# Performance work log

Hardware: AMD Instinct MI355X
Metric: run time of the kernel (lower is better)

Reference implementation:

```python
import jax, jax.numpy as jnp
import numpy as np
from jax import lax

DIM, HEADS, HIDDEN = 384, 6, 1536
B, D, H, W = 2, 14, 14, 14
LN_EPS = 1e-5


def setup_inputs() -> dict:
    key = jax.random.key(0)
    ks = jax.random.split(key, 8)
    s = 0.02
    return {
        "x": jax.random.normal(ks[0], (B, DIM, D, H, W), jnp.float32),
        "conv_w": jax.random.normal(ks[1], (DIM, 1, 3, 3, 3), jnp.float32) * s,
        "conv_b": jnp.zeros((DIM,), jnp.float32),
        "ln1_w": jnp.ones((DIM,), jnp.float32),
        "ln1_b": jnp.zeros((DIM,), jnp.float32),
        "qkv_w": jax.random.normal(ks[2], (3 * DIM, DIM), jnp.float32) * s,
        "proj_w": jax.random.normal(ks[3], (DIM, DIM), jnp.float32) * s,
        "proj_b": jnp.zeros((DIM,), jnp.float32),
        "ln2_w": jnp.ones((DIM,), jnp.float32),
        "ln2_b": jnp.zeros((DIM,), jnp.float32),
        "fc1_w": jax.random.normal(ks[4], (HIDDEN, DIM), jnp.float32) * s,
        "fc1_b": jnp.zeros((HIDDEN,), jnp.float32),
        "fc2_w": jax.random.normal(ks[5], (DIM, HIDDEN), jnp.float32) * s,
        "fc2_b": jnp.zeros((DIM,), jnp.float32),
    }


def _layernorm(x, w, b):
    mu = jnp.mean(x, axis=-1, keepdims=True)
    var = jnp.var(x, axis=-1, keepdims=True)
    return (x - mu) * lax.rsqrt(var + LN_EPS) * w + b


def reference(x, conv_w, conv_b, ln1_w, ln1_b, qkv_w, proj_w, proj_b,
              ln2_w, ln2_b, fc1_w, fc1_b, fc2_w, fc2_b):
    Bn, C = x.shape[0], x.shape[1]
    Dd, Hh, Ww = x.shape[2], x.shape[3], x.shape[4]
    # depthwise conv3d positional embedding (groups=dim), padding=1
    pos = lax.conv_general_dilated(
        x, conv_w, window_strides=(1, 1, 1), padding="SAME",
        feature_group_count=C,
        dimension_numbers=("NCDHW", "OIDHW", "NCDHW"))
    x = x + pos + conv_b[None, :, None, None, None] * 0 + conv_b[None, :, None, None, None]
    # fix: bias belongs to conv output only once
    x = x - conv_b[None, :, None, None, None]
    N = Dd * Hh * Ww
    t = x.reshape(Bn, C, N).transpose(0, 2, 1)  # [B, N, C]

    # attention
    hd = C // HEADS
    scale = hd ** -0.5
    tn = _layernorm(t, ln1_w, ln1_b)
    qkv = tn @ qkv_w.T  # [B, N, 3C]
    qkv = qkv.reshape(Bn, N, 3, HEADS, hd).transpose(2, 0, 3, 1, 4)
    q, k, v = qkv[0], qkv[1], qkv[2]  # [B, H, N, hd]
    attn = jax.nn.softmax(jnp.einsum("bhnd,bhmd->bhnm", q, k) * scale, axis=-1)
    o = jnp.einsum("bhnm,bhmd->bhnd", attn, v)
    o = o.transpose(0, 2, 1, 3).reshape(Bn, N, C)
    t = t + o @ proj_w.T + proj_b

    # MLP (exact GELU, matching torch nn.GELU default)
    tn2 = _layernorm(t, ln2_w, ln2_b)
    h = jax.nn.gelu(tn2 @ fc1_w.T + fc1_b, approximate=False)
    t = t + h @ fc2_w.T + fc2_b

    return t.transpose(0, 2, 1).reshape(Bn, C, Dd, Hh, Ww)
```

## Files before the change

### kernel.cpp

```cpp
#include <hip/hip_runtime.h>
#include <hip/hip_bf16.h>
#include <math.h>

#define DIM 384
#define HEADS 6
#define HIDDEN 1536
#define NTOK 2744
#define BATCH 2
#define MTOT (BATCH * NTOK)
#define KSPLIT 4
#define NQT 22
#define CEXP 0.18033688f

typedef __bf16 bf16x8 __attribute__((ext_vector_type(8)));
typedef __bf16 bf16x4 __attribute__((ext_vector_type(4)));
typedef float  f32x4  __attribute__((ext_vector_type(4)));

#define F_GELU  1
#define F_RESID 2
#define F_BF16  4
#define F_QKV   8
#define F_TRANS 16

__device__ __forceinline__ void gll16(const void* g, void* l) {
    __builtin_amdgcn_global_load_lds(
        (const __attribute__((address_space(1))) unsigned int*)g,
        (__attribute__((address_space(3))) unsigned int*)l, 16, 0, 0);
}

__global__ void k_conv(const float* __restrict__ x, const float* __restrict__ cw,
                       float* __restrict__ t,
                       const float* __restrict__ w0, const float* __restrict__ w1,
                       const float* __restrict__ w2, const float* __restrict__ w3,
                       __bf16* o0, __bf16* o1, __bf16* o2, __bf16* o3) {
    int bid = blockIdx.x;
    if (bid >= 528) {
        int i = (bid - 528) * 256 + threadIdx.x;
        const float* s; __bf16* d; int off;
        if (i < 110592)      { s = w0; d = o0; off = i; }
        else if (i < 147456) { s = w1; d = o1; off = i - 110592; }
        else if (i < 294912) { s = w2; d = o2; off = i - 147456; }
        else                 { s = w3; d = o3; off = i - 294912; }
        float4 v = ((const float4*)s)[off];
        bf16x4 bb = { (__bf16)v.x, (__bf16)v.y, (__bf16)v.z, (__bf16)v.w };
        *(bf16x4*)(d + (size_t)off * 4) = bb;
        return;
    }
    int nb = bid % 11, rest = bid / 11;
    int cb = rest % 24, b = rest / 24;
    int c0 = cb * 16;
    int n = nb * 256 + threadIdx.x;
    if (n >= NTOK) return;
    int d = n / 196, r = n % 196, h = r / 14, w = r % 14;
    const float* xb = x + ((size_t)b * DIM + c0) * NTOK;
    float acc[16];
    #pragma unroll
    for (int c = 0; c < 16; c++) acc[c] = xb[(size_t)c * NTOK + n];
    #pragma unroll
    for (int kd = 0; kd < 3; kd++) {
        int dd = d + kd - 1;
        if (dd < 0 || dd >= 14) continue;
        #pragma unroll
        for (int kh = 0; kh < 3; kh++) {
            int hh = h + kh - 1;
            if (hh < 0 || hh >= 14) continue;
            #pragma unroll
            for (int kw = 0; kw < 3; kw++) {
                int ww = w + kw - 1;
                if (ww < 0 || ww >= 14) continue;
                int np = (dd * 14 + hh) * 14 + ww;
                int tap = kd * 9 + kh * 3 + kw;
                #pragma unroll
                for (int c = 0; c < 16; c++)
                    acc[c] = fmaf(cw[(c0 + c) * 27 + tap], xb[(size_t)c * NTOK + np], acc[c]);
            }
        }
    }
    float* tp = t + (size_t)(b * NTOK + n) * DIM + c0;
    #pragma unroll
    for (int c = 0; c < 16; c += 4) {
        float4 v = { acc[c], acc[c + 1], acc[c + 2], acc[c + 3] };
        *(float4*)(tp + c) = v;
    }
}

__device__ __forceinline__ void ln_body(const float* __restrict__ in,
                                        __bf16* __restrict__ out,
                                        const float* __restrict__ w,
                                        const float* __restrict__ b) {
    int wid = threadIdx.x >> 6, lane = threadIdx.x & 63;
    int token = blockIdx.x * 4 + wid;
    const float* row = in + (size_t)token * DIM;
    float v[6], s = 0.f, s2 = 0.f;
    #pragma unroll
    for (int i = 0; i < 6; i++) {
        v[i] = row[lane + 64 * i];
        s += v[i]; s2 += v[i] * v[i];
    }
    #pragma unroll
    for (int m = 1; m < 64; m <<= 1) { s += __shfl_xor(s, m); s2 += __shfl_xor(s2, m); }
    float mu = s * (1.f / DIM);
    float rstd = rsqrtf(s2 * (1.f / DIM) - mu * mu + 1e-5f);
    __bf16* orow = out + (size_t)token * DIM;
    #pragma unroll
    for (int i = 0; i < 6; i++) {
        int c = lane + 64 * i;
        orow[c] = (__bf16)((v[i] - mu) * rstd * w[c] + b[c]);
    }
}
__global__ void k_ln1(const float* in, __bf16* out, const float* w, const float* b) {
    ln_body(in, out, w, b);
}
__global__ void k_ln2(const float* in, __bf16* out, const float* w, const float* b) {
    ln_body(in, out, w, b);
}

__device__ __forceinline__ void gemm12864_body(
    const __bf16* __restrict__ A, const __bf16* __restrict__ B,
    const float* __restrict__ bias, void* __restrict__ out,
    __bf16* __restrict__ vt_out, int M, int N, int K, int flags) {
    __shared__ __bf16 As[128][64];
    __shared__ __bf16 Bs[64][64];
    int tid = threadIdx.x, lane = tid & 63, wid = tid >> 6;
    int quad = lane >> 4, l16 = lane & 15;
    int wm = wid & 1, wn = wid >> 1;
    int m0 = blockIdx.y * 128, n0 = blockIdx.x * 64;
    int x7 = l16 & 7;

    auto stage = [&](int k0) {
        #pragma unroll
        for (int i = 0; i < 4; i++) {
            int c = i * 256 + tid;
            int row = c >> 3, cc = (c & 7) ^ (row & 7);
            int gm = m0 + row; if (gm > M - 1) gm = M - 1;
            gll16(A + (size_t)gm * K + k0 + cc * 8, &As[0][0] + (size_t)c * 8);
        }
        #pragma unroll
        for (int i = 0; i < 2; i++) {
            int c = i * 256 + tid;
            int row = c >> 3, cc = (c & 7) ^ (row & 7);
            gll16(B + (size_t)(n0 + row) * K + k0 + cc * 8, &Bs[0][0] + (size_t)c * 8);
        }
    };

    f32x4 acc[4][2] = {};
    int nk = K >> 6;
    for (int ki = 0; ki < nk; ki++) {
        if (ki) __syncthreads();
        stage(ki << 6);
        __syncthreads();
        #pragma unroll
        for (int s = 0; s < 2; s++) {
            bf16x8 a[4], b[2];
            #pragma unroll
            for (int i = 0; i < 4; i++)
                a[i] = *(bf16x8*)&As[wm * 64 + i * 16 + l16][(((s * 4 + quad) ^ x7)) * 8];
            #pragma unroll
            for (int j = 0; j < 2; j++)
                b[j] = *(bf16x8*)&Bs[wn * 32 + j * 16 + l16][(((s * 4 + quad) ^ x7)) * 8];
            #pragma unroll
            for (int i = 0; i < 4; i++)
                #pragma unroll
                for (int j = 0; j < 2; j++)
                    acc[i][j] = __builtin_amdgcn_mfma_f32_16x16x32_bf16(a[i], b[j], acc[i][j], 0, 0, 0);
        }
    }

    int colb = n0 + wn * 32;
    #pragma unroll
    for (int j = 0; j < 2; j++) {
        int col = colb + j * 16 + l16;
        float bv = bias ? bias[col] : 0.f;
        #pragma unroll
        for (int i = 0; i < 4; i++) {
            int row0 = m0 + wm * 64 + i * 16 + quad * 4;
            if (row0 >= M) continue;
            float v4[4];
            #pragma unroll
            for (int r = 0; r < 4; r++) {
                float v = acc[i][j][r] + bv;
                if (flags & F_GELU) v = 0.5f * v * (1.f + erff(v * 0.70710678f));
                if ((flags & F_QKV) && col < 384) v *= CEXP;
                v4[r] = v;
            }
            if ((flags & F_QKV) && col >= 768) {
                int b2 = row0 / NTOK, n2 = row0 - b2 * NTOK;
                bf16x4 pk = { (__bf16)v4[0], (__bf16)v4[1], (__bf16)v4[2], (__bf16)v4[3] };
                *(bf16x4*)(vt_out + ((size_t)(b2 * DIM + (col - 768))) * NTOK + n2) = pk;
            } else {
                #pragma unroll
                for (int r = 0; r < 4; r++)
                    ((__bf16*)out)[(size_t)(row0 + r) * N + col] = (__bf16)v4[r];
            }
        }
    }
}
__global__ __launch_bounds__(256) void k_qkv(const __bf16* A, const __bf16* B,
        void* out, __bf16* vt_out, int M, int N, int K) {
    gemm12864_body(A, B, nullptr, out, vt_out, M, N, K, F_QKV);
}
__global__ __launch_bounds__(256) void k_fc1(const __bf16* A, const __bf16* B,
        const float* bias, void* out, int M, int N, int K) {
    gemm12864_body(A, B, bias, out, nullptr, M, N, K, F_GELU | F_BF16);
}

__device__ __forceinline__ void gemm64_body(
    const __bf16* __restrict__ A, const __bf16* __restrict__ B,
    const float* __restrict__ bias, const float* __restrict__ resid,
    void* __restrict__ out, int M, int N, int K, int flags) {
    __shared__ __align__(16) char sm[17408];
    __bf16 (*As)[64] = (__bf16(*)[64])sm;
    __bf16 (*Bs)[64] = (__bf16(*)[64])(sm + 8192);
    float* Tt = (float*)sm;
    int tid = threadIdx.x, lane = tid & 63, wid = tid >> 6;
    int quad = lane >> 4, l16 = lane & 15;
    int wm = wid & 1, wn = wid >> 1;
    int m0 = blockIdx.y * 64, n0 = blockIdx.x * 64;
    int x7 = l16 & 7;

    auto stage = [&](int k0) {
        #pragma unroll
        for (int i = 0; i < 2; i++) {
            int c = i * 256 + tid;
            int row = c >> 3, cc = (c & 7) ^ (row & 7);
            int gm = m0 + row; if (gm > M - 1) gm = M - 1;
            gll16(A + (size_t)gm * K + k0 + cc * 8, &As[0][0] + (size_t)c * 8);
        }
        #pragma unroll
        for (int i = 0; i < 2; i++) {
            int c = i * 256 + tid;
            int row = c >> 3, cc = (c & 7) ^ (row & 7);
            gll16(B + (size_t)(n0 + row) * K + k0 + cc * 8, &Bs[0][0] + (size_t)c * 8);
        }
    };

    f32x4 acc[2][2] = {};
    int nk = K >> 6;
    for (int ki = 0; ki < nk; ki++) {
        if (ki) __syncthreads();
        stage(ki << 6);
        __syncthreads();
        #pragma unroll
        for (int s = 0; s < 2; s++) {
            bf16x8 a[2], b[2];
            #pragma unroll
            for (int i = 0; i < 2; i++)
                a[i] = *(bf16x8*)&As[wm * 32 + i * 16 + l16][(((s * 4 + quad) ^ x7)) * 8];
            #pragma unroll
            for (int j = 0; j < 2; j++)
                b[j] = *(bf16x8*)&Bs[wn * 32 + j * 16 + l16][(((s * 4 + quad) ^ x7)) * 8];
            #pragma unroll
            for (int i = 0; i < 2; i++)
                #pragma unroll
                for (int j = 0; j < 2; j++)
                    acc[i][j] = __builtin_amdgcn_mfma_f32_16x16x32_bf16(a[i], b[j], acc[i][j], 0, 0, 0);
        }
    }

    if (flags & F_TRANS) {
        #pragma unroll
        for (int half = 0; half < 2; half++) {
            __syncthreads();
            if (wn == half) {
                #pragma unroll
                for (int j = 0; j < 2; j++) {
                    int colL = j * 16 + l16;
                    int col = n0 + half * 32 + colL;
                    float bv = bias[col];
                    #pragma unroll
                    for (int i = 0; i < 2; i++) {
                        int rowL = wm * 32 + i * 16 + quad * 4;
                        float v4[4];
                        #pragma unroll
                        for (int r = 0; r < 4; r++) {
                            int rr = m0 + rowL + r; if (rr > M - 1) rr = M - 1;
                            v4[r] = acc[i][j][r] + bv + resid[(size_t)rr * N + col];
                        }
                        float4 pk = { v4[0], v4[1], v4[2], v4[3] };
                        *(float4*)&Tt[colL * 68 + rowL] = pk;
                    }
                }
            }
            __syncthreads();
            int c = tid >> 3, no = (tid & 7) * 8;
            int col = n0 + half * 32 + c;
            #pragma unroll
            for (int q2 = 0; q2 < 2; q2++) {
                int nn = no + q2 * 4;
                int row = m0 + nn;
                if (row >= M) continue;
                int b2 = row / NTOK, n2 = row - b2 * NTOK;
                float4 v = *(float4*)&Tt[c * 68 + nn];
                *(float4*)((float*)out + ((size_t)(b2 * N + col)) * NTOK + n2) = v;
            }
        }
        return;
    }

    #pragma unroll
    for (int j = 0; j < 2; j++) {
        int col = n0 + wn * 32 + j * 16 + l16;
        float bv = bias ? bias[col] : 0.f;
        #pragma unroll
        for (int i = 0; i < 2; i++) {
            int row0 = m0 + wm * 32 + i * 16 + quad * 4;
            if (row0 >= M) continue;
            #pragma unroll
            for (int r = 0; r < 4; r++) {
                float v = acc[i][j][r] + bv;
                if (flags & F_RESID) v += resid[(size_t)(row0 + r) * N + col];
                ((float*)out)[(size_t)(row0 + r) * N + col] = v;
            }
        }
    }
}
__global__ __launch_bounds__(256) void k_proj(const __bf16* A, const __bf16* B,
        const float* bias, const float* resid, void* out, int M, int N, int K) {
    gemm64_body(A, B, bias, resid, out, M, N, K, F_RESID);
}
__global__ __launch_bounds__(256) void k_fc2(const __bf16* A, const __bf16* B,
        const float* bias, const float* resid, void* out, int M, int N, int K) {
    gemm64_body(A, B, bias, resid, out, M, N, K, F_RESID | F_TRANS);
}

__global__ __launch_bounds__(512, 8) void k_attn(const __bf16* __restrict__ qkv,
                                                 const __bf16* __restrict__ vt,
                                                 __bf16* __restrict__ opart,
                                                 float* __restrict__ lpart) {
    __shared__ __align__(16) __bf16 KV[2][2][64][64];
    __bf16 (*Qs)[64] = (__bf16(*)[64])KV;

    int tid = threadIdx.x, lane = tid & 63, wid = tid >> 6;
    int quad = lane >> 4, l16 = lane & 15;
    int q0 = blockIdx.x * 128;
    int bh = blockIdx.y;
    int ks = blockIdx.z;
    int b = bh / HEADS, h = bh % HEADS;
    int x7 = l16 & 7;

    int kt0 = (43 * ks) / KSPLIT, kt1 = (43 * (ks + 1)) / KSPLIT;

    int srow = tid >> 3, scc = (tid & 7) ^ (srow & 7);
    const __bf16* pK = qkv + ((size_t)(b * NTOK + kt0 * 64 + srow)) * 1152 + 384 + h * 64 + scc * 8;
    const __bf16* pV = vt + ((size_t)(bh * 64 + srow)) * NTOK + kt0 * 64 + scc * 8;

    auto stageKV = [&](int kt, int bufi) {
        const __bf16* kp = pK + (size_t)(kt - kt0) * (64 * 1152);
        if (kt == 42 && srow >= 56)
            kp = qkv + ((size_t)(b * NTOK + NTOK - 1)) * 1152 + 384 + h * 64 + scc * 8;
        gll16(kp, &KV[bufi][0][0][0] + (size_t)tid * 8);
        gll16(pV + (size_t)(kt - kt0) * 64, &KV[bufi][1][0][0] + (size_t)tid * 8);
    };

    #pragma unroll
    for (int i = 0; i < 2; i++) {
        int c = i * 512 + tid;
        int row = c >> 3, cc = (c & 7) ^ (row & 7);
        int gq = q0 + row; if (gq > NTOK - 1) gq = NTOK - 1;
        gll16(qkv + ((size_t)(b * NTOK + gq)) * 1152 + h * 64 + cc * 8,
              &Qs[0][0] + (size_t)c * 8);
    }
    __syncthreads();

    bf16x8 aq[2];
    #pragma unroll
    for (int sx = 0; sx < 2; sx++)
        aq[sx] = *(bf16x8*)&Qs[wid * 16 + l16][((sx * 4 + quad) ^ x7) * 8];
    __syncthreads();

    stageKV(kt0, 0);

    int koff0 = (quad ^ x7) * 8, koff1 = ((4 + quad) ^ x7) * 8;
    int voffl[2], voffh[2];
    #pragma unroll
    for (int sx = 0; sx < 2; sx++) {
        voffl[sx] = ((4 * sx + (quad >> 1)) ^ x7) * 8 + (quad & 1) * 4;
        voffh[sx] = ((4 * sx + 2 + (quad >> 1)) ^ x7) * 8 + (quad & 1) * 4;
    }

    const f32x4 fzero = {0.f, 0.f, 0.f, 0.f};
    f32x4 oaccT[4] = {};
    float l_sum = 0.f;

    int bufi = 0;
    for (int kt = kt0; kt < kt1; kt++) {
        __syncthreads();
        if (kt + 1 < kt1) stageKV(kt + 1, bufi ^ 1);

        const __bf16* ksb = &KV[bufi][0][0][0] + l16 * 64;
        const __bf16* vtb = &KV[bufi][1][0][0] + l16 * 64;
        bool tail = (kt == 42);

        bf16x8 pb[2];
        #pragma unroll
        for (int t = 0; t < 4; t++) {
            bf16x8 bk0 = *(bf16x8*)(ksb + t * 1024 + koff0);
            bf16x8 bk1 = *(bf16x8*)(ksb + t * 1024 + koff1);
            f32x4 z = __builtin_amdgcn_mfma_f32_16x16x32_bf16(bk0, aq[0], fzero, 0, 0, 0);
            z = __builtin_amdgcn_mfma_f32_16x16x32_bf16(bk1, aq[1], z, 0, 0, 0);
            float e0 = exp2f(z[0]), e1 = exp2f(z[1]), e2 = exp2f(z[2]), e3 = exp2f(z[3]);
            if (tail) {
                int kb = kt * 64 + t * 16 + quad * 4;
                if (kb + 0 >= NTOK) e0 = 0.f;
                if (kb + 1 >= NTOK) e1 = 0.f;
                if (kb + 2 >= NTOK) e2 = 0.f;
                if (kb + 3 >= NTOK) e3 = 0.f;
            }
            l_sum += (e0 + e1) + (e2 + e3);
            int half = (t & 1) * 4, px = t >> 1;
            pb[px][half + 0] = (__bf16)e0;
            pb[px][half + 1] = (__bf16)e1;
            pb[px][half + 2] = (__bf16)e2;
            pb[px][half + 3] = (__bf16)e3;
        }

        #pragma unroll
        for (int dt = 0; dt < 4; dt++) {
            const __bf16* vr = vtb + dt * 1024;
            #pragma unroll
            for (int sx = 0; sx < 2; sx++) {
                bf16x4 lo = *(bf16x4*)(vr + voffl[sx]);
                bf16x4 hi = *(bf16x4*)(vr + voffh[sx]);
                bf16x8 av = { lo[0], lo[1], lo[2], lo[3],
                              hi[0], hi[1], hi[2], hi[3] };
                oaccT[dt] = __builtin_amdgcn_mfma_f32_16x16x32_bf16(av, pb[sx], oaccT[dt], 0, 0, 0);
            }
        }
        bufi ^= 1;
    }

    float l = l_sum;
    l += __shfl_xor(l, 16);
    l += __shfl_xor(l, 32);
    int gq = q0 + wid * 16 + l16;
    if (quad == 0 && gq < NTOK)
        lpart[((size_t)ks * 12 + bh) * NTOK + gq] = l;

    if (gq < NTOK) {
        __bf16* op = opart + ((size_t)ks * MTOT + (size_t)b * NTOK + gq) * DIM + h * 64;
        #pragma unroll
        for (int dt = 0; dt < 4; dt++) {
            bf16x4 pk = { (__bf16)oaccT[dt][0], (__bf16)oaccT[dt][1],
                          (__bf16)oaccT[dt][2], (__bf16)oaccT[dt][3] };
            *(bf16x4*)(op + dt * 16 + quad * 4) = pk;
        }
    }
}

__global__ void k_comb(const __bf16* __restrict__ opart,
                       const float* __restrict__ lpart,
                       __bf16* __restrict__ o) {
    int idx = blockIdx.x * 256 + threadIdx.x;
    int token = idx / 96, rem = idx - token * 96;
    int c = rem * 4, h = c >> 6;
    int b2 = token / NTOK, n = token - b2 * NTOK;
    int bh = b2 * HEADS + h;
    float a0 = 0.f, a1 = 0.f, a2 = 0.f, a3 = 0.f, l = 0.f;
    #pragma unroll
    for (int ks = 0; ks < KSPLIT; ks++) {
        bf16x4 p = *(const bf16x4*)&opart[((size_t)ks * MTOT + token) * DIM + c];
        a0 += (float)p[0]; a1 += (float)p[1]; a2 += (float)p[2]; a3 += (float)p[3];
        l += lpart[((size_t)ks * 12 + bh) * NTOK + n];
    }
    float inv = 1.f / l;
    bf16x4 ov = { (__bf16)(a0 * inv), (__bf16)(a1 * inv),
                  (__bf16)(a2 * inv), (__bf16)(a3 * inv) };
    *(bf16x4*)(o + (size_t)token * DIM + c) = ov;
}

extern "C" void kernel_launch(void* const* d_in, const int* in_sizes, int n_in,
                              void* d_out, int out_size, void* d_ws, size_t ws_size,
                              hipStream_t stream) {
    const float* x      = (const float*)d_in[0];
    const float* conv_w = (const float*)d_in[1];
    const float* ln1_w  = (const float*)d_in[3];
    const float* ln1_b  = (const float*)d_in[4];
    const float* qkv_w  = (const float*)d_in[5];
    const float* proj_w = (const float*)d_in[6];
    const float* proj_b = (const float*)d_in[7];
    const float* ln2_w  = (const float*)d_in[8];
    const float* ln2_b  = (const float*)d_in[9];
    const float* fc1_w  = (const float*)d_in[10];
    const float* fc1_b  = (const float*)d_in[11];
    const float* fc2_w  = (const float*)d_in[12];
    const float* fc2_b  = (const float*)d_in[13];
    float* out = (float*)d_out;

    char* p = (char*)d_ws;
    float*  T    = (float*)p;  p += (size_t)MTOT * DIM * 4;
    __bf16* TN   = (__bf16*)p; p += (size_t)MTOT * DIM * 2;
    __bf16* QKV  = (__bf16*)p; p += (size_t)MTOT * 1152 * 2;
    __bf16* VT   = (__bf16*)p; p += (size_t)BATCH * DIM * NTOK * 2;
    __bf16* O    = (__bf16*)p; p += (size_t)MTOT * DIM * 2;
    __bf16* H    = (__bf16*)p; p += (size_t)MTOT * HIDDEN * 2;
    __bf16* WQ   = (__bf16*)p; p += (size_t)1152 * 384 * 2;
    __bf16* WP   = (__bf16*)p; p += (size_t)384 * 384 * 2;
    __bf16* W1   = (__bf16*)p; p += (size_t)1536 * 384 * 2;
    __bf16* W2   = (__bf16*)p; p += (size_t)384 * 1536 * 2;
    float*  LP   = (float*)p;  p += (size_t)KSPLIT * 12 * NTOK * 4;
    __bf16* OP   = (__bf16*)p; p += (size_t)KSPLIT * MTOT * DIM * 2;

    k_conv<<<528 + 1728, 256, 0, stream>>>(
        x, conv_w, T, qkv_w, proj_w, fc1_w, fc2_w, WQ, WP, W1, W2);
    k_ln1<<<MTOT / 4, 256, 0, stream>>>(T, TN, ln1_w, ln1_b);
    k_qkv<<<dim3(18, 43), 256, 0, stream>>>(TN, WQ, QKV, VT, MTOT, 1152, 384);
    k_attn<<<dim3(NQT, 12, KSPLIT), 512, 0, stream>>>(QKV, VT, OP, LP);
    k_comb<<<(MTOT * 96) / 256, 256, 0, stream>>>(OP, LP, O);
    k_proj<<<dim3(6, 86), 256, 0, stream>>>(O, WP, proj_b, T, T, MTOT, 384, 384);
    k_ln2<<<MTOT / 4, 256, 0, stream>>>(T, TN, ln2_w, ln2_b);
    k_fc1<<<dim3(24, 43), 256, 0, stream>>>(TN, W1, fc1_b, H, MTOT, 1536, 384);
    k_fc2<<<dim3(6, 86), 256, 0, stream>>>(H, W2, fc2_b, T, out, MTOT, 384, 1536);
}
```

Before: 248.2 us.

## Double attention query tile per block, pre-permute V^T, XCD-aware block mapping

Each attention block now handles 256 queries (two 16-row tiles per wave), so every K/V tile staged in shared memory is reused across twice as many queries. The QKV GEMM writes V^T padded to 2752 columns with a permuted token order, letting the PV MFMA operand load as one contiguous bf16x8 instead of two bf16x4 pieces. Padding columns are zeroed in the conv kernel. Blocks are launched on a flat grid remapped so that blocks sharing a (batch, head, split) land on the same XCD, and partial outputs are stored in a lane-native layout that the combine kernel reads back. The cost is more registers per thread (occupancy hint lowered to 4) and half as many query blocks.

```diff
diff --git a/kernel.cpp b/kernel.cpp
--- a/kernel.cpp
+++ b/kernel.cpp
@@ -6,10 +6,11 @@
 #define HEADS 6
 #define HIDDEN 1536
 #define NTOK 2744
+#define NTOKP 2752
 #define BATCH 2
 #define MTOT (BATCH * NTOK)
 #define KSPLIT 4
-#define NQT 22
+#define NQT 11
 #define CEXP 0.18033688f
 
 typedef __bf16 bf16x8 __attribute__((ext_vector_type(8)));
@@ -32,8 +33,19 @@
                        float* __restrict__ t,
                        const float* __restrict__ w0, const float* __restrict__ w1,
                        const float* __restrict__ w2, const float* __restrict__ w3,
-                       __bf16* o0, __bf16* o1, __bf16* o2, __bf16* o3) {
+                       __bf16* o0, __bf16* o1, __bf16* o2, __bf16* o3,
+                       __bf16* vt_pad) {
     int bid = blockIdx.x;
+    if (bid >= 2256) {
+        #pragma unroll
+        for (int k = 0; k < 6; k++) {
+            int idx = k * 256 + threadIdx.x;
+            int row = idx >> 1, half = idx & 1;
+            bf16x4 z4 = { (__bf16)0.f, (__bf16)0.f, (__bf16)0.f, (__bf16)0.f };
+            *(bf16x4*)(vt_pad + (size_t)row * NTOKP + 2732 + half * 16) = z4;
+        }
+        return;
+    }
     if (bid >= 528) {
         int i = (bid - 528) * 256 + threadIdx.x;
         const float* s; __bf16* d; int off;
@@ -185,8 +197,9 @@
             }
             if ((flags & F_QKV) && col >= 768) {
                 int b2 = row0 / NTOK, n2 = row0 - b2 * NTOK;
+                int n2p = (n2 & ~63) | (((n2 >> 2) & 3) << 4) | (((n2 >> 4) & 3) << 2);
                 bf16x4 pk = { (__bf16)v4[0], (__bf16)v4[1], (__bf16)v4[2], (__bf16)v4[3] };
-                *(bf16x4*)(vt_out + ((size_t)(b2 * DIM + (col - 768))) * NTOK + n2) = pk;
+                *(bf16x4*)(vt_out + ((size_t)(b2 * DIM + (col - 768))) * NTOKP + n2p) = pk;
             } else {
                 #pragma unroll
                 for (int r = 0; r < 4; r++)
@@ -323,7 +336,7 @@
     gemm64_body(A, B, bias, resid, out, M, N, K, F_RESID | F_TRANS);
 }
 
-__global__ __launch_bounds__(512, 8) void k_attn(const __bf16* __restrict__ qkv,
+__global__ __launch_bounds__(512, 4) void k_attn(const __bf16* __restrict__ qkv,
                                                  const __bf16* __restrict__ vt,
                                                  __bf16* __restrict__ opart,
                                                  float* __restrict__ lpart) {
@@ -332,9 +345,12 @@
 
     int tid = threadIdx.x, lane = tid & 63, wid = tid >> 6;
     int quad = lane >> 4, l16 = lane & 15;
-    int q0 = blockIdx.x * 128;
-    int bh = blockIdx.y;
-    int ks = blockIdx.z;
+    int flat = blockIdx.x;
+    int xcd = flat & 7, slot = flat >> 3;
+    int grp = slot / 11, qb = slot - grp * 11;
+    int g = xcd + 8 * grp;
+    int bh = g % 12, ks = g / 12;
+    int q0 = qb * 256;
     int b = bh / HEADS, h = bh % HEADS;
     int x7 = l16 & 7;
 
@@ -342,7 +358,7 @@
 
     int srow = tid >> 3, scc = (tid & 7) ^ (srow & 7);
     const __bf16* pK = qkv + ((size_t)(b * NTOK + kt0 * 64 + srow)) * 1152 + 384 + h * 64 + scc * 8;
-    const __bf16* pV = vt + ((size_t)(bh * 64 + srow)) * NTOK + kt0 * 64 + scc * 8;
+    const __bf16* pV = vt + ((size_t)(bh * 64 + srow)) * NTOKP + kt0 * 64 + scc * 8;
 
     auto stageKV = [&](int kt, int bufi) {
         const __bf16* kp = pK + (size_t)(kt - kt0) * (64 * 1152);
@@ -353,7 +369,7 @@
     };
 
     #pragma unroll
-    for (int i = 0; i < 2; i++) {
+    for (int i = 0; i < 4; i++) {
         int c = i * 512 + tid;
         int row = c >> 3, cc = (c & 7) ^ (row & 7);
         int gq = q0 + row; if (gq > NTOK - 1) gq = NTOK - 1;
@@ -362,25 +378,22 @@
     }
     __syncthreads();
 
-    bf16x8 aq[2];
-    #pragma unroll
-    for (int sx = 0; sx < 2; sx++)
-        aq[sx] = *(bf16x8*)&Qs[wid * 16 + l16][((sx * 4 + quad) ^ x7) * 8];
+    bf16x8 aq[2][2];
+    #pragma unroll
+    for (int qt = 0; qt < 2; qt++)
+        #pragma unroll
+        for (int sx = 0; sx < 2; sx++)
+            aq[qt][sx] = *(bf16x8*)&Qs[wid * 32 + qt * 16 + l16][((sx * 4 + quad) ^ x7) * 8];
     __syncthreads();
 
     stageKV(kt0, 0);
 
     int koff0 = (quad ^ x7) * 8, koff1 = ((4 + quad) ^ x7) * 8;
-    int voffl[2], voffh[2];
-    #pragma unroll
-    for (int sx = 0; sx < 2; sx++) {
-        voffl[sx] = ((4 * sx + (quad >> 1)) ^ x7) * 8 + (quad & 1) * 4;
-        voffh[sx] = ((4 * sx + 2 + (quad >> 1)) ^ x7) * 8 + (quad & 1) * 4;
-    }
+    int voff0 = ((quad * 2 + 0) ^ x7) * 8, voff1 = ((quad * 2 + 1) ^ x7) * 8;
 
     const f32x4 fzero = {0.f, 0.f, 0.f, 0.f};
-    f32x4 oaccT[4] = {};
-    float l_sum = 0.f;
+    f32x4 oaccT[2][4] = {};
+    float l_sum[2] = {0.f, 0.f};
 
     int bufi = 0;
     for (int kt = kt0; kt < kt1; kt++) {
@@ -391,60 +404,65 @@
         const __bf16* vtb = &KV[bufi][1][0][0] + l16 * 64;
         bool tail = (kt == 42);
 
-        bf16x8 pb[2];
+        bf16x8 pb[2][2];
         #pragma unroll
         for (int t = 0; t < 4; t++) {
             bf16x8 bk0 = *(bf16x8*)(ksb + t * 1024 + koff0);
             bf16x8 bk1 = *(bf16x8*)(ksb + t * 1024 + koff1);
-            f32x4 z = __builtin_amdgcn_mfma_f32_16x16x32_bf16(bk0, aq[0], fzero, 0, 0, 0);
-            z = __builtin_amdgcn_mfma_f32_16x16x32_bf16(bk1, aq[1], z, 0, 0, 0);
-            float e0 = exp2f(z[0]), e1 = exp2f(z[1]), e2 = exp2f(z[2]), e3 = exp2f(z[3]);
-            if (tail) {
-                int kb = kt * 64 + t * 16 + quad * 4;
-                if (kb + 0 >= NTOK) e0 = 0.f;
-                if (kb + 1 >= NTOK) e1 = 0.f;
-                if (kb + 2 >= NTOK) e2 = 0.f;
-                if (kb + 3 >= NTOK) e3 = 0.f;
-            }
-            l_sum += (e0 + e1) + (e2 + e3);
-            int half = (t & 1) * 4, px = t >> 1;
-            pb[px][half + 0] = (__bf16)e0;
-            pb[px][half + 1] = (__bf16)e1;
-            pb[px][half + 2] = (__bf16)e2;
-            pb[px][half + 3] = (__bf16)e3;
+            #pragma unroll
+            for (int qt = 0; qt < 2; qt++) {
+                f32x4 z = __builtin_amdgcn_mfma_f32_16x16x32_bf16(bk0, aq[qt][0], fzero, 0, 0, 0);
+                z = __builtin_amdgcn_mfma_f32_16x16x32_bf16(bk1, aq[qt][1], z, 0, 0, 0);
+                float e0 = exp2f(z[0]), e1 = exp2f(z[1]), e2 = exp2f(z[2]), e3 = exp2f(z[3]);
+                if (tail) {
+                    int kb = kt * 64 + t * 16 + quad * 4;
+                    if (kb + 0 >= NTOK) e0 = 0.f;
+                    if (kb + 1 >= NTOK) e1 = 0.f;
+                    if (kb + 2 >= NTOK) e2 = 0.f;
+                    if (kb + 3 >= NTOK) e3 = 0.f;
+                }
+                l_sum[qt] += (e0 + e1) + (e2 + e3);
+                int half = (t & 1) * 4, px = t >> 1;
+                pb[qt][px][half + 0] = (__bf16)e0;
+                pb[qt][px][half + 1] = (__bf16)e1;
+                pb[qt][px][half + 2] = (__bf16)e2;
+                pb[qt][px][half + 3] = (__bf16)e3;
+            }
         }
 
         #pragma unroll
         for (int dt = 0; dt < 4; dt++) {
             const __bf16* vr = vtb + dt * 1024;
-            #pragma unroll
-            for (int sx = 0; sx < 2; sx++) {
-                bf16x4 lo = *(bf16x4*)(vr + voffl[sx]);
-                bf16x4 hi = *(bf16x4*)(vr + voffh[sx]);
-                bf16x8 av = { lo[0], lo[1], lo[2], lo[3],
-                              hi[0], hi[1], hi[2], hi[3] };
-                oaccT[dt] = __builtin_amdgcn_mfma_f32_16x16x32_bf16(av, pb[sx], oaccT[dt], 0, 0, 0);
+            bf16x8 av0 = *(bf16x8*)(vr + voff0);
+            bf16x8 av1 = *(bf16x8*)(vr + voff1);
+            #pragma unroll
+            for (int qt = 0; qt < 2; qt++) {
+                oaccT[qt][dt] = __builtin_amdgcn_mfma_f32_16x16x32_bf16(av0, pb[qt][0], oaccT[qt][dt], 0, 0, 0);
+                oaccT[qt][dt] = __builtin_amdgcn_mfma_f32_16x16x32_bf16(av1, pb[qt][1], oaccT[qt][dt], 0, 0, 0);
             }
         }
         bufi ^= 1;
     }
 
-    float l = l_sum;
-    l += __shfl_xor(l, 16);
-    l += __shfl_xor(l, 32);
-    int gq = q0 + wid * 16 + l16;
-    if (quad == 0 && gq < NTOK)
-        lpart[((size_t)ks * 12 + bh) * NTOK + gq] = l;
-
-    if (gq < NTOK) {
-        __bf16* op = opart + ((size_t)ks * MTOT + (size_t)b * NTOK + gq) * DIM + h * 64;
+    #pragma unroll
+    for (int qt = 0; qt < 2; qt++) {
+        float l = l_sum[qt];
+        l += __shfl_xor(l, 16);
+        l += __shfl_xor(l, 32);
+        int gq = q0 + wid * 32 + qt * 16 + l16;
+        if (quad == 0 && gq < NTOK)
+            lpart[((size_t)ks * 12 + bh) * NTOK + gq] = l;
+    }
+
+    __bf16* op = opart + ((((size_t)(ks * 12 + bh) * 11 + qb) * 8 + wid) * 2048);
+    #pragma unroll
+    for (int qt = 0; qt < 2; qt++)
         #pragma unroll
         for (int dt = 0; dt < 4; dt++) {
-            bf16x4 pk = { (__bf16)oaccT[dt][0], (__bf16)oaccT[dt][1],
-                          (__bf16)oaccT[dt][2], (__bf16)oaccT[dt][3] };
-            *(bf16x4*)(op + dt * 16 + quad * 4) = pk;
-        }
-    }
+            bf16x4 pk = { (__bf16)oaccT[qt][dt][0], (__bf16)oaccT[qt][dt][1],
+                          (__bf16)oaccT[qt][dt][2], (__bf16)oaccT[qt][dt][3] };
+            *(bf16x4*)(op + ((qt * 4 + dt) * 64 + lane) * 4) = pk;
+        }
 }
 
 __global__ void k_comb(const __bf16* __restrict__ opart,
@@ -455,10 +473,16 @@
     int c = rem * 4, h = c >> 6;
     int b2 = token / NTOK, n = token - b2 * NTOK;
     int bh = b2 * HEADS + h;
+    int qb = n >> 8, nb = n & 255;
+    int wid = nb >> 5, qt = (nb >> 4) & 1, l16 = nb & 15;
+    int ch = c & 63, dt = ch >> 4, quad = (ch >> 2) & 3;
+    int lane = quad * 16 + l16;
+    size_t gbase = ((((size_t)bh * 11 + qb) * 8 + wid) * 512 + (qt * 4 + dt) * 64 + lane) * 4;
+    const size_t kstride = (size_t)12 * 11 * 8 * 2048;
     float a0 = 0.f, a1 = 0.f, a2 = 0.f, a3 = 0.f, l = 0.f;
     #pragma unroll
     for (int ks = 0; ks < KSPLIT; ks++) {
-        bf16x4 p = *(const bf16x4*)&opart[((size_t)ks * MTOT + token) * DIM + c];
+        bf16x4 p = *(const bf16x4*)&opart[(size_t)ks * kstride + gbase];
         a0 += (float)p[0]; a1 += (float)p[1]; a2 += (float)p[2]; a3 += (float)p[3];
         l += lpart[((size_t)ks * 12 + bh) * NTOK + n];
     }
@@ -490,7 +514,7 @@
     float*  T    = (float*)p;  p += (size_t)MTOT * DIM * 4;
     __bf16* TN   = (__bf16*)p; p += (size_t)MTOT * DIM * 2;
     __bf16* QKV  = (__bf16*)p; p += (size_t)MTOT * 1152 * 2;
-    __bf16* VT   = (__bf16*)p; p += (size_t)BATCH * DIM * NTOK * 2;
+    __bf16* VT   = (__bf16*)p; p += (size_t)BATCH * DIM * NTOKP * 2;
     __bf16* O    = (__bf16*)p; p += (size_t)MTOT * DIM * 2;
     __bf16* H    = (__bf16*)p; p += (size_t)MTOT * HIDDEN * 2;
     __bf16* WQ   = (__bf16*)p; p += (size_t)1152 * 384 * 2;
@@ -498,13 +522,13 @@
     __bf16* W1   = (__bf16*)p; p += (size_t)1536 * 384 * 2;
     __bf16* W2   = (__bf16*)p; p += (size_t)384 * 1536 * 2;
     float*  LP   = (float*)p;  p += (size_t)KSPLIT * 12 * NTOK * 4;
-    __bf16* OP   = (__bf16*)p; p += (size_t)KSPLIT * MTOT * DIM * 2;
-
-    k_conv<<<528 + 1728, 256, 0, stream>>>(
-        x, conv_w, T, qkv_w, proj_w, fc1_w, fc2_w, WQ, WP, W1, W2);
+    __bf16* OP   = (__bf16*)p; p += (size_t)KSPLIT * 12 * 11 * 8 * 2048 * 2;
+
+    k_conv<<<528 + 1728 + 1, 256, 0, stream>>>(
+        x, conv_w, T, qkv_w, proj_w, fc1_w, fc2_w, WQ, WP, W1, W2, VT);
     k_ln1<<<MTOT / 4, 256, 0, stream>>>(T, TN, ln1_w, ln1_b);
     k_qkv<<<dim3(18, 43), 256, 0, stream>>>(TN, WQ, QKV, VT, MTOT, 1152, 384);
-    k_attn<<<dim3(NQT, 12, KSPLIT), 512, 0, stream>>>(QKV, VT, OP, LP);
+    k_attn<<<528, 512, 0, stream>>>(QKV, VT, OP, LP);
     k_comb<<<(MTOT * 96) / 256, 256, 0, stream>>>(OP, LP, O);
     k_proj<<<dim3(6, 86), 256, 0, stream>>>(O, WP, proj_b, T, T, MTOT, 384, 384);
     k_ln2<<<MTOT / 4, 256, 0, stream>>>(T, TN, ln2_w, ln2_b);
```

After: 236.1 us. 4.9% less time.

## Pad and permute V^T layout, remap attention blocks per XCD, tile partial outputs

Applied to the files above, without the earlier changes.

Pads the V-transpose buffer to a 64-aligned token stride and permutes token order within each 64-block, so the attention PV MFMA operands become single 16-byte LDS reads instead of two 8-byte halves. An extra conv block zeroes the pad tail. The attention grid is flattened and remapped so blocks sharing a (batch, head, k-split) group land on the same XCD, which should improve L2 reuse of K/V. Partial outputs are written in a lane-contiguous tiled layout that k_comb indexes back into, giving coalesced stores, at the cost of more complex index arithmetic in the combine step.

```diff
diff --git a/kernel.cpp b/kernel.cpp
--- a/kernel.cpp
+++ b/kernel.cpp
@@ -6,10 +6,11 @@
 #define HEADS 6
 #define HIDDEN 1536
 #define NTOK 2744
+#define NTOKP 2752
 #define BATCH 2
 #define MTOT (BATCH * NTOK)
 #define KSPLIT 4
-#define NQT 22
+#define NQB 22
 #define CEXP 0.18033688f
 
 typedef __bf16 bf16x8 __attribute__((ext_vector_type(8)));
@@ -32,8 +33,19 @@
                        float* __restrict__ t,
                        const float* __restrict__ w0, const float* __restrict__ w1,
                        const float* __restrict__ w2, const float* __restrict__ w3,
-                       __bf16* o0, __bf16* o1, __bf16* o2, __bf16* o3) {
+                       __bf16* o0, __bf16* o1, __bf16* o2, __bf16* o3,
+                       __bf16* vt_pad) {
     int bid = blockIdx.x;
+    if (bid >= 2256) {
+        #pragma unroll
+        for (int k = 0; k < 6; k++) {
+            int idx = k * 256 + threadIdx.x;
+            int row = idx >> 1, half = idx & 1;
+            bf16x4 z4 = { (__bf16)0.f, (__bf16)0.f, (__bf16)0.f, (__bf16)0.f };
+            *(bf16x4*)(vt_pad + (size_t)row * NTOKP + 2732 + half * 16) = z4;
+        }
+        return;
+    }
     if (bid >= 528) {
         int i = (bid - 528) * 256 + threadIdx.x;
         const float* s; __bf16* d; int off;
@@ -185,8 +197,9 @@
             }
             if ((flags & F_QKV) && col >= 768) {
                 int b2 = row0 / NTOK, n2 = row0 - b2 * NTOK;
+                int n2p = (n2 & ~63) | (((n2 >> 2) & 3) << 4) | (((n2 >> 4) & 3) << 2);
                 bf16x4 pk = { (__bf16)v4[0], (__bf16)v4[1], (__bf16)v4[2], (__bf16)v4[3] };
-                *(bf16x4*)(vt_out + ((size_t)(b2 * DIM + (col - 768))) * NTOK + n2) = pk;
+                *(bf16x4*)(vt_out + ((size_t)(b2 * DIM + (col - 768))) * NTOKP + n2p) = pk;
             } else {
                 #pragma unroll
                 for (int r = 0; r < 4; r++)
@@ -332,9 +345,12 @@
 
     int tid = threadIdx.x, lane = tid & 63, wid = tid >> 6;
     int quad = lane >> 4, l16 = lane & 15;
-    int q0 = blockIdx.x * 128;
-    int bh = blockIdx.y;
-    int ks = blockIdx.z;
+    int flat = blockIdx.x;
+    int xcd = flat & 7, slot = flat >> 3;
+    int grp = slot / NQB, qb = slot - grp * NQB;
+    int g = xcd + 8 * grp;
+    int bh = g % 12, ks = g / 12;
+    int q0 = qb * 128;
     int b = bh / HEADS, h = bh % HEADS;
     int x7 = l16 & 7;
 
@@ -342,7 +358,7 @@
 
     int srow = tid >> 3, scc = (tid & 7) ^ (srow & 7);
     const __bf16* pK = qkv + ((size_t)(b * NTOK + kt0 * 64 + srow)) * 1152 + 384 + h * 64 + scc * 8;
-    const __bf16* pV = vt + ((size_t)(bh * 64 + srow)) * NTOK + kt0 * 64 + scc * 8;
+    const __bf16* pV = vt + ((size_t)(bh * 64 + srow)) * NTOKP + kt0 * 64 + scc * 8;
 
     auto stageKV = [&](int kt, int bufi) {
         const __bf16* kp = pK + (size_t)(kt - kt0) * (64 * 1152);
@@ -371,12 +387,7 @@
     stageKV(kt0, 0);
 
     int koff0 = (quad ^ x7) * 8, koff1 = ((4 + quad) ^ x7) * 8;
-    int voffl[2], voffh[2];
-    #pragma unroll
-    for (int sx = 0; sx < 2; sx++) {
-        voffl[sx] = ((4 * sx + (quad >> 1)) ^ x7) * 8 + (quad & 1) * 4;
-        voffh[sx] = ((4 * sx + 2 + (quad >> 1)) ^ x7) * 8 + (quad & 1) * 4;
-    }
+    int voff0 = ((quad * 2 + 0) ^ x7) * 8, voff1 = ((quad * 2 + 1) ^ x7) * 8;
 
     const f32x4 fzero = {0.f, 0.f, 0.f, 0.f};
     f32x4 oaccT[4] = {};
@@ -417,14 +428,10 @@
         #pragma unroll
         for (int dt = 0; dt < 4; dt++) {
             const __bf16* vr = vtb + dt * 1024;
-            #pragma unroll
-            for (int sx = 0; sx < 2; sx++) {
-                bf16x4 lo = *(bf16x4*)(vr + voffl[sx]);
-                bf16x4 hi = *(bf16x4*)(vr + voffh[sx]);
-                bf16x8 av = { lo[0], lo[1], lo[2], lo[3],
-                              hi[0], hi[1], hi[2], hi[3] };
-                oaccT[dt] = __builtin_amdgcn_mfma_f32_16x16x32_bf16(av, pb[sx], oaccT[dt], 0, 0, 0);
-            }
+            bf16x8 av0 = *(bf16x8*)(vr + voff0);
+            bf16x8 av1 = *(bf16x8*)(vr + voff1);
+            oaccT[dt] = __builtin_amdgcn_mfma_f32_16x16x32_bf16(av0, pb[0], oaccT[dt], 0, 0, 0);
+            oaccT[dt] = __builtin_amdgcn_mfma_f32_16x16x32_bf16(av1, pb[1], oaccT[dt], 0, 0, 0);
         }
         bufi ^= 1;
     }
@@ -436,14 +443,12 @@
     if (quad == 0 && gq < NTOK)
         lpart[((size_t)ks * 12 + bh) * NTOK + gq] = l;
 
-    if (gq < NTOK) {
-        __bf16* op = opart + ((size_t)ks * MTOT + (size_t)b * NTOK + gq) * DIM + h * 64;
-        #pragma unroll
-        for (int dt = 0; dt < 4; dt++) {
-            bf16x4 pk = { (__bf16)oaccT[dt][0], (__bf16)oaccT[dt][1],
-                          (__bf16)oaccT[dt][2], (__bf16)oaccT[dt][3] };
-            *(bf16x4*)(op + dt * 16 + quad * 4) = pk;
-        }
+    __bf16* op = opart + ((((size_t)(ks * 12 + bh) * NQB + qb) * 8 + wid) * 1024);
+    #pragma unroll
+    for (int dt = 0; dt < 4; dt++) {
+        bf16x4 pk = { (__bf16)oaccT[dt][0], (__bf16)oaccT[dt][1],
+                      (__bf16)oaccT[dt][2], (__bf16)oaccT[dt][3] };
+        *(bf16x4*)(op + (dt * 64 + lane) * 4) = pk;
     }
 }
 
@@ -455,10 +460,16 @@
     int c = rem * 4, h = c >> 6;
     int b2 = token / NTOK, n = token - b2 * NTOK;
     int bh = b2 * HEADS + h;
+    int qb = n >> 7, nb = n & 127;
+    int wid = nb >> 4, l16 = nb & 15;
+    int ch = c & 63, dt = ch >> 4, quad = (ch >> 2) & 3;
+    int lane = quad * 16 + l16;
+    size_t gbase = (((size_t)bh * NQB + qb) * 8 + wid) * 1024 + (dt * 64 + lane) * 4;
+    const size_t kstride = (size_t)12 * NQB * 8 * 1024;
     float a0 = 0.f, a1 = 0.f, a2 = 0.f, a3 = 0.f, l = 0.f;
     #pragma unroll
     for (int ks = 0; ks < KSPLIT; ks++) {
-        bf16x4 p = *(const bf16x4*)&opart[((size_t)ks * MTOT + token) * DIM + c];
+        bf16x4 p = *(const bf16x4*)&opart[(size_t)ks * kstride + gbase];
         a0 += (float)p[0]; a1 += (float)p[1]; a2 += (float)p[2]; a3 += (float)p[3];
         l += lpart[((size_t)ks * 12 + bh) * NTOK + n];
     }
@@ -490,7 +501,7 @@
     float*  T    = (float*)p;  p += (size_t)MTOT * DIM * 4;
     __bf16* TN   = (__bf16*)p; p += (size_t)MTOT * DIM * 2;
     __bf16* QKV  = (__bf16*)p; p += (size_t)MTOT * 1152 * 2;
-    __bf16* VT   = (__bf16*)p; p += (size_t)BATCH * DIM * NTOK * 2;
+    __bf16* VT   = (__bf16*)p; p += (size_t)BATCH * DIM * NTOKP * 2;
     __bf16* O    = (__bf16*)p; p += (size_t)MTOT * DIM * 2;
     __bf16* H    = (__bf16*)p; p += (size_t)MTOT * HIDDEN * 2;
     __bf16* WQ   = (__bf16*)p; p += (size_t)1152 * 384 * 2;
@@ -498,13 +509,13 @@
     __bf16* W1   = (__bf16*)p; p += (size_t)1536 * 384 * 2;
     __bf16* W2   = (__bf16*)p; p += (size_t)384 * 1536 * 2;
     float*  LP   = (float*)p;  p += (size_t)KSPLIT * 12 * NTOK * 4;
-    __bf16* OP   = (__bf16*)p; p += (size_t)KSPLIT * MTOT * DIM * 2;
-
-    k_conv<<<528 + 1728, 256, 0, stream>>>(
-        x, conv_w, T, qkv_w, proj_w, fc1_w, fc2_w, WQ, WP, W1, W2);
+    __bf16* OP   = (__bf16*)p; p += (size_t)KSPLIT * 12 * NQB * 8 * 1024 * 2;
+
+    k_conv<<<528 + 1728 + 1, 256, 0, stream>>>(
+        x, conv_w, T, qkv_w, proj_w, fc1_w, fc2_w, WQ, WP, W1, W2, VT);
     k_ln1<<<MTOT / 4, 256, 0, stream>>>(T, TN, ln1_w, ln1_b);
     k_qkv<<<dim3(18, 43), 256, 0, stream>>>(TN, WQ, QKV, VT, MTOT, 1152, 384);
-    k_attn<<<dim3(NQT, 12, KSPLIT), 512, 0, stream>>>(QKV, VT, OP, LP);
+    k_attn<<<NQB * 12 * KSPLIT, 512, 0, stream>>>(QKV, VT, OP, LP);
     k_comb<<<(MTOT * 96) / 256, 256, 0, stream>>>(OP, LP, O);
     k_proj<<<dim3(6, 86), 256, 0, stream>>>(O, WP, proj_b, T, T, MTOT, 384, 384);
     k_ln2<<<MTOT / 4, 256, 0, stream>>>(T, TN, ln2_w, ln2_b);
```

Result: faster. 231.6 us (-6.7%).
